# Kernel optimization log

Measured on AMD Instinct MI355X. Metric: run time of the kernel, lower is better.

## Reference

```python
import jax, jax.numpy as jnp
import numpy as np
from jax import lax

H, W = 4096, 4096

def setup_inputs() -> dict:
    key = jax.random.key(0)
    k_occ, k_seed = jax.random.split(key)
    occupied = (jax.random.uniform(k_occ, (H, W)) < 0.3).astype(jnp.float32)
    flood = ((jax.random.uniform(k_seed, (H, W)) < 1e-3).astype(jnp.float32)
             * (1.0 - occupied))
    flood_input = jnp.stack([occupied, flood], axis=-1)  # [H, W, 2]
    flood_count = jnp.zeros((H, W), dtype=jnp.float32)
    # Fixed flood kernel, HWIO layout: (3, 3, in=2, out=1)
    kernel = jnp.zeros((3, 3, 2, 1), dtype=jnp.float32)
    kernel = kernel.at[1, 1, 0, 0].set(-5.0)  # occupied center blocks flood
    kernel = kernel.at[1, 2, 1, 0].set(1.0)   # right
    kernel = kernel.at[2, 1, 1, 0].set(1.0)   # down
    kernel = kernel.at[1, 0, 1, 0].set(1.0)   # left
    kernel = kernel.at[0, 1, 1, 0].set(1.0)   # up
    kernel = kernel.at[1, 1, 1, 0].set(1.0)   # center
    bias = jnp.zeros((1,), dtype=jnp.float32)
    return {"flood_input": flood_input, "flood_count": flood_count,
            "kernel": kernel, "bias": bias, "num_steps": 16}

def reference(flood_input, flood_count, kernel, bias, num_steps):
    dn = ("NHWC", "HWIO", "NHWC")

    def flood_step(carry, _):
        x, count = carry                      # x: [H, W, 2], count: [H, W]
        occupied = x[..., 0]
        y = lax.conv_general_dilated(x[None], kernel, (1, 1), "SAME",
                                     dimension_numbers=dn)[0, ..., 0] + bias[0]
        y = jnp.clip(y, 0.0, 1.0)             # flooded frontier
        new_x = jnp.stack([occupied, y], axis=-1)
        return (new_x, count + y), None

    (x_final, count_final), _ = lax.scan(flood_step,
                                         (flood_input, flood_count),
                                         None, length=num_steps)
    # [H, W, 3]: occupied, flood, count
    return jnp.concatenate([x_final, count_final[..., None]], axis=-1)
```

## Files before the change

kernel.cpp:

```cpp
#include <hip/hip_runtime.h>


typedef unsigned long long u64;

#define HH 4096
#define WW 4096
#define WPR 64
#define TILE 96
#define HALO 16
#define REG 128
#define NSTEPS 16

__global__ __launch_bounds__(256) void pack_kernel(
    const float* __restrict__ flood_input,
    u64* __restrict__ occP, u64* __restrict__ flP)
{
    const int lane = threadIdx.x & 63;
    const int wv   = threadIdx.x >> 6;
    const int r    = blockIdx.x;
#pragma unroll
    for (int b = 0; b < 2; ++b) {
        float vx[8], vy[8];
#pragma unroll
        for (int j = 0; j < 8; ++j) {
            const int w = wv * 16 + b * 8 + j;
            const float2 v = *(const float2*)(flood_input +
                                ((size_t)r * WW + (w << 6) + lane) * 2);
            vx[j] = v.x; vy[j] = v.y;
        }
#pragma unroll
        for (int j = 0; j < 8; ++j) {
            const int w = wv * 16 + b * 8 + j;
            const u64 om = __ballot(vx[j] > 0.5f);
            const u64 fm = __ballot(vy[j] > 0.5f);
            if (lane == 0) {
                occP[(size_t)r * WPR + w] = om;
                flP [(size_t)r * WPR + w] = fm;
            }
        }
    }
}

__global__ __launch_bounds__(256, 8) void flood_kernel(
    const u64* __restrict__ occP, const u64* __restrict__ flP,
    const float* __restrict__ flood_count,
    float* __restrict__ out)
{
    __shared__ u64 occL[REG * 2];
    __shared__ u64 bufA[REG * 2];
    __shared__ u64 bufB[REG * 2];
    __shared__ u64 cntL[TILE * 2 * 5];

    const int tid  = threadIdx.x;
    const int lane = tid & 63;
    const int wv   = tid >> 6;

    const int tile_r0 = blockIdx.y * TILE;
    const int tile_c0 = blockIdx.x * TILE;
    const int row0 = tile_r0 - HALO;
    const int col0 = tile_c0 - HALO;

    const int r  = tid >> 1, h = tid & 1;
    const int gr = row0 + r;
    const bool rin = (gr >= 0) & (gr < HH);
    const int s  = col0 + (h << 6);
    const int q0 = ((s + 64) >> 6) - 1;
    const int sh = s - (q0 << 6);

    const size_t base = (size_t)(rin ? gr : 0) * WPR;
    const int qa = min(max(q0, 0), WPR - 1);
    const int qb = min(max(q0 + 1, 0), WPR - 1);
    u64 o0 = occP[base + qa], o1 = occP[base + qb];
    u64 f0 = flP [base + qa], f1 = flP [base + qb];
    const bool va = rin & (q0 >= 0);
    const bool vb = rin & (q0 + 1 < WPR);
    if (!va) { o0 = ~0ull; f0 = 0ull; }
    if (!vb) { o1 = ~0ull; f1 = 0ull; }
    const u64 occ = (o0 >> sh) | (sh ? (o1 << (64 - sh)) : 0ull);
    u64       f   = (f0 >> sh) | (sh ? (f1 << (64 - sh)) : 0ull);

    occL[tid] = occ;
    bufA[tid] = f;
    __syncthreads();

    u64 cnt0 = 0, cnt1 = 0, cnt2 = 0, cnt3 = 0, cnt4 = 0;
    const u64 nocc = ~occ;
    u64* cur = bufA;
    u64* nxt = bufB;
    for (int it = 0; it < NSTEPS; ++it) {
        const u64 up = (r > 0)       ? cur[tid - 2] : 0ull;
        const u64 dn = (r < REG - 1) ? cur[tid + 2] : 0ull;
        const u64 nb = cur[tid ^ 1];
        const u64 cl = h ? (nb >> 63) : 0ull;
        const u64 cr = h ? 0ull : (nb << 63);
        const u64 nf = nocc & (f | (f << 1) | cl | (f >> 1) | cr | up | dn);
        u64 c = nf, t;
        t = cnt0; cnt0 = t ^ c; c = t & c;
        t = cnt1; cnt1 = t ^ c; c = t & c;
        t = cnt2; cnt2 = t ^ c; c = t & c;
        t = cnt3; cnt3 = t ^ c; c = t & c;
        cnt4 ^= c;
        nxt[tid] = nf;
        f = nf;
        __syncthreads();
        u64* tmp = cur; cur = nxt; nxt = tmp;
    }

    if (r >= HALO && r < HALO + TILE) {
        const int rr = r - HALO;
        u64* c = &cntL[(rr * 2 + h) * 5];
        c[0] = cnt0; c[1] = cnt1; c[2] = cnt2; c[3] = cnt3; c[4] = cnt4;
    }
    __syncthreads();

#pragma unroll 2
    for (int orow = wv; orow < TILE; orow += 4) {
        const int grr = tile_r0 + orow;
        if (grr >= HH) continue;
        const int gc0 = tile_c0 + lane;
        const int gc1 = tile_c0 + 64 + lane;
        const bool v0 = gc0 < WW;
        const bool v1 = (lane < 32) && (gc1 < WW);
        const float fc0 = v0 ? flood_count[(size_t)grr * WW + gc0] : 0.f;
        const float fc1 = v1 ? flood_count[(size_t)grr * WW + gc1] : 0.f;
        const int rreg = orow + HALO;
#pragma unroll
        for (int sp = 0; sp < 2; ++sp) {
            const bool vv = sp ? v1 : v0;
            if (!vv) continue;
            const int oc  = (sp << 6) + lane;
            const int gc  = sp ? gc1 : gc0;
            const int creg = oc + HALO;
            const int word = creg >> 6, bit = creg & 63;
            const u64 ow = occL[rreg * 2 + word];
            const u64 fw = cur [rreg * 2 + word];
            const u64* cp = &cntL[(orow * 2 + word) * 5];
            int cv = 0;
#pragma unroll
            for (int k = 0; k < 5; ++k)
                cv += (int)((cp[k] >> bit) & 1ull) << k;
            float3 o3;
            o3.x = (float)((ow >> bit) & 1ull);
            o3.y = (float)((fw >> bit) & 1ull);
            o3.z = (float)cv + (sp ? fc1 : fc0);
            *(float3*)(out + ((size_t)grr * WW + gc) * 3) = o3;
        }
    }
}

extern "C" void kernel_launch(void* const* d_in, const int* in_sizes, int n_in,
                              void* d_out, int out_size, void* d_ws, size_t ws_size,
                              hipStream_t stream) {
    const float* flood_input = (const float*)d_in[0];
    const float* flood_cnt   = (const float*)d_in[1];
    float* out = (float*)d_out;

    u64* occP = (u64*)d_ws;
    u64* flP  = occP + (size_t)HH * WPR;

    pack_kernel<<<dim3(HH), dim3(256), 0, stream>>>(flood_input, occP, flP);

    dim3 grid((WW + TILE - 1) / TILE, (HH + TILE - 1) / TILE);
    flood_kernel<<<grid, dim3(256), 0, stream>>>(occP, flP, flood_cnt, out);
}
```

Measured before the change: 381.9 us.

## Split flood into column-strip bit-plane kernel and separate expand kernel

Measured after the change: 389.5 us. No clear change (+2.0%).

```diff
diff --git a/kernel.cpp b/kernel.cpp
--- a/kernel.cpp
+++ b/kernel.cpp
@@ -6,14 +6,12 @@
 #define HH 4096
 #define WW 4096
 #define WPR 64
-#define TILE 96
-#define HALO 16
-#define REG 128
 #define NSTEPS 16
+#define VROWS 224
+#define RROWS 256
 
 __global__ __launch_bounds__(256) void pack_kernel(
-    const float* __restrict__ flood_input,
-    u64* __restrict__ occP, u64* __restrict__ flP)
+    const float* __restrict__ in, u64* __restrict__ occP, u64* __restrict__ flP)
 {
     const int lane = threadIdx.x & 63;
     const int wv   = threadIdx.x >> 6;
@@ -24,8 +22,7 @@
 #pragma unroll
         for (int j = 0; j < 8; ++j) {
             const int w = wv * 16 + b * 8 + j;
-            const float2 v = *(const float2*)(flood_input +
-                                ((size_t)r * WW + (w << 6) + lane) * 2);
+            const float2 v = *(const float2*)(in + ((size_t)r * WW + (w << 6) + lane) * 2);
             vx[j] = v.x; vy[j] = v.y;
         }
 #pragma unroll
@@ -34,117 +31,116 @@
             const u64 om = __ballot(vx[j] > 0.5f);
             const u64 fm = __ballot(vy[j] > 0.5f);
             if (lane == 0) {
-                occP[(size_t)r * WPR + w] = om;
-                flP [(size_t)r * WPR + w] = fm;
+                occP[(size_t)w * HH + r] = om;
+                flP [(size_t)w * HH + r] = fm;
             }
         }
     }
 }
 
-__global__ __launch_bounds__(256, 8) void flood_kernel(
+__global__ __launch_bounds__(256) void flood_kernel(
     const u64* __restrict__ occP, const u64* __restrict__ flP,
-    const float* __restrict__ flood_count,
-    float* __restrict__ out)
+    u64* __restrict__ planes)
 {
-    __shared__ u64 occL[REG * 2];
-    __shared__ u64 bufA[REG * 2];
-    __shared__ u64 bufB[REG * 2];
-    __shared__ u64 cntL[TILE * 2 * 5];
+    __shared__ u64 bufA[RROWS * 2];
+    __shared__ u64 bufB[RROWS * 2];
 
-    const int tid  = threadIdx.x;
-    const int lane = tid & 63;
-    const int wv   = tid >> 6;
+    const int tid = threadIdx.x;
+    const int w   = blockIdx.x;
+    const int gr  = blockIdx.y * VROWS + tid - 16;
+    const bool rin = (gr >= 0) && (gr < HH);
 
-    const int tile_r0 = blockIdx.y * TILE;
-    const int tile_c0 = blockIdx.x * TILE;
-    const int row0 = tile_r0 - HALO;
-    const int col0 = tile_c0 - HALO;
+    u64 oc[3], fl[3];
+#pragma unroll
+    for (int j = 0; j < 3; ++j) {
+        const int q = w - 1 + j;
+        const bool v = rin && (q >= 0) && (q < WPR);
+        oc[j] = v ? occP[(size_t)q * HH + gr] : ~0ull;
+        fl[j] = v ? flP [(size_t)q * HH + gr] : 0ull;
+    }
+    const u64 nocc0 = ~((oc[0] >> 48) | (oc[1] << 16));
+    const u64 nocc1 = ~((oc[1] >> 48) | (oc[2] << 16));
+    u64 f0 = (fl[0] >> 48) | (fl[1] << 16);
+    u64 f1 = (fl[1] >> 48) | (fl[2] << 16);
 
-    const int r  = tid >> 1, h = tid & 1;
-    const int gr = row0 + r;
-    const bool rin = (gr >= 0) & (gr < HH);
-    const int s  = col0 + (h << 6);
-    const int q0 = ((s + 64) >> 6) - 1;
-    const int sh = s - (q0 << 6);
+    u64 c00 = 0, c01 = 0, c02 = 0, c03 = 0, c04 = 0;
+    u64 c10 = 0, c11 = 0, c12 = 0, c13 = 0, c14 = 0;
 
-    const size_t base = (size_t)(rin ? gr : 0) * WPR;
-    const int qa = min(max(q0, 0), WPR - 1);
-    const int qb = min(max(q0 + 1, 0), WPR - 1);
-    u64 o0 = occP[base + qa], o1 = occP[base + qb];
-    u64 f0 = flP [base + qa], f1 = flP [base + qb];
-    const bool va = rin & (q0 >= 0);
-    const bool vb = rin & (q0 + 1 < WPR);
-    if (!va) { o0 = ~0ull; f0 = 0ull; }
-    if (!vb) { o1 = ~0ull; f1 = 0ull; }
-    const u64 occ = (o0 >> sh) | (sh ? (o1 << (64 - sh)) : 0ull);
-    u64       f   = (f0 >> sh) | (sh ? (f1 << (64 - sh)) : 0ull);
-
-    occL[tid] = occ;
-    bufA[tid] = f;
+    bufA[tid * 2 + 0] = f0; bufA[tid * 2 + 1] = f1;
     __syncthreads();
 
-    u64 cnt0 = 0, cnt1 = 0, cnt2 = 0, cnt3 = 0, cnt4 = 0;
-    const u64 nocc = ~occ;
     u64* cur = bufA;
     u64* nxt = bufB;
     for (int it = 0; it < NSTEPS; ++it) {
-        const u64 up = (r > 0)       ? cur[tid - 2] : 0ull;
-        const u64 dn = (r < REG - 1) ? cur[tid + 2] : 0ull;
-        const u64 nb = cur[tid ^ 1];
-        const u64 cl = h ? (nb >> 63) : 0ull;
-        const u64 cr = h ? 0ull : (nb << 63);
-        const u64 nf = nocc & (f | (f << 1) | cl | (f >> 1) | cr | up | dn);
-        u64 c = nf, t;
-        t = cnt0; cnt0 = t ^ c; c = t & c;
-        t = cnt1; cnt1 = t ^ c; c = t & c;
-        t = cnt2; cnt2 = t ^ c; c = t & c;
-        t = cnt3; cnt3 = t ^ c; c = t & c;
-        cnt4 ^= c;
-        nxt[tid] = nf;
-        f = nf;
+        u64 up0 = 0, up1 = 0, dn0 = 0, dn1 = 0;
+        if (tid > 0)         { up0 = cur[(tid - 1) * 2 + 0]; up1 = cur[(tid - 1) * 2 + 1]; }
+        if (tid < RROWS - 1) { dn0 = cur[(tid + 1) * 2 + 0]; dn1 = cur[(tid + 1) * 2 + 1]; }
+        const u64 nf0 = nocc0 & (f0 | (f0 << 1) | (f0 >> 1) | (f1 << 63) | up0 | dn0);
+        const u64 nf1 = nocc1 & (f1 | (f1 << 1) | (f0 >> 63) | (f1 >> 1) | up1 | dn1);
+        u64 c, t;
+        c = nf0;
+        t = c00; c00 = t ^ c; c = t & c;
+        t = c01; c01 = t ^ c; c = t & c;
+        t = c02; c02 = t ^ c; c = t & c;
+        t = c03; c03 = t ^ c; c = t & c;
+        c04 ^= c;
+        c = nf1;
+        t = c10; c10 = t ^ c; c = t & c;
+        t = c11; c11 = t ^ c; c = t & c;
+        t = c12; c12 = t ^ c; c = t & c;
+        t = c13; c13 = t ^ c; c = t & c;
+        c14 ^= c;
+        nxt[tid * 2 + 0] = nf0; nxt[tid * 2 + 1] = nf1;
+        f0 = nf0; f1 = nf1;
         __syncthreads();
         u64* tmp = cur; cur = nxt; nxt = tmp;
     }
 
-    if (r >= HALO && r < HALO + TILE) {
-        const int rr = r - HALO;
-        u64* c = &cntL[(rr * 2 + h) * 5];
-        c[0] = cnt0; c[1] = cnt1; c[2] = cnt2; c[3] = cnt3; c[4] = cnt4;
+    if (tid >= 16 && tid < 16 + VROWS && gr < HH) {
+        const size_t o = (size_t)w * HH + gr;
+        const size_t P = (size_t)WPR * HH;
+        planes[o]         = (f0  >> 16) | (f1  << 48);
+        planes[P + o]     = (c00 >> 16) | (c10 << 48);
+        planes[2 * P + o] = (c01 >> 16) | (c11 << 48);
+        planes[3 * P + o] = (c02 >> 16) | (c12 << 48);
+        planes[4 * P + o] = (c03 >> 16) | (c13 << 48);
+        planes[5 * P + o] = (c04 >> 16) | (c14 << 48);
     }
-    __syncthreads();
+}
+
+__global__ __launch_bounds__(256) void expand_kernel(
+    const u64* __restrict__ occP, const u64* __restrict__ planes,
+    const float* __restrict__ fcount, float* __restrict__ out)
+{
+    const int lane = threadIdx.x & 63;
+    const int wv   = threadIdx.x >> 6;
+    const int w    = blockIdx.x;
+    const int r0   = blockIdx.y * 64 + wv * 16;
+    const size_t P = (size_t)WPR * HH;
+    const size_t col = (size_t)(w << 6) + lane;
 
 #pragma unroll 2
-    for (int orow = wv; orow < TILE; orow += 4) {
-        const int grr = tile_r0 + orow;
-        if (grr >= HH) continue;
-        const int gc0 = tile_c0 + lane;
-        const int gc1 = tile_c0 + 64 + lane;
-        const bool v0 = gc0 < WW;
-        const bool v1 = (lane < 32) && (gc1 < WW);
-        const float fc0 = v0 ? flood_count[(size_t)grr * WW + gc0] : 0.f;
-        const float fc1 = v1 ? flood_count[(size_t)grr * WW + gc1] : 0.f;
-        const int rreg = orow + HALO;
-#pragma unroll
-        for (int sp = 0; sp < 2; ++sp) {
-            const bool vv = sp ? v1 : v0;
-            if (!vv) continue;
-            const int oc  = (sp << 6) + lane;
-            const int gc  = sp ? gc1 : gc0;
-            const int creg = oc + HALO;
-            const int word = creg >> 6, bit = creg & 63;
-            const u64 ow = occL[rreg * 2 + word];
-            const u64 fw = cur [rreg * 2 + word];
-            const u64* cp = &cntL[(orow * 2 + word) * 5];
-            int cv = 0;
-#pragma unroll
-            for (int k = 0; k < 5; ++k)
-                cv += (int)((cp[k] >> bit) & 1ull) << k;
-            float3 o3;
-            o3.x = (float)((ow >> bit) & 1ull);
-            o3.y = (float)((fw >> bit) & 1ull);
-            o3.z = (float)cv + (sp ? fc1 : fc0);
-            *(float3*)(out + ((size_t)grr * WW + gc) * 3) = o3;
-        }
+    for (int i = 0; i < 16; ++i) {
+        const int r = r0 + i;
+        const size_t o = (size_t)w * HH + r;
+        const u64 ow = occP[o];
+        const u64 fw = planes[o];
+        const u64 q0 = planes[P + o];
+        const u64 q1 = planes[2 * P + o];
+        const u64 q2 = planes[3 * P + o];
+        const u64 q3 = planes[4 * P + o];
+        const u64 q4 = planes[5 * P + o];
+        const float fc = fcount[(size_t)r * WW + col];
+        const int cv = (int)((q0 >> lane) & 1ull)
+                     + ((int)((q1 >> lane) & 1ull) << 1)
+                     + ((int)((q2 >> lane) & 1ull) << 2)
+                     + ((int)((q3 >> lane) & 1ull) << 3)
+                     + ((int)((q4 >> lane) & 1ull) << 4);
+        float3 o3;
+        o3.x = (float)((ow >> lane) & 1ull);
+        o3.y = (float)((fw >> lane) & 1ull);
+        o3.z = (float)cv + fc;
+        *(float3*)(out + ((size_t)r * WW + col) * 3) = o3;
     }
 }
 
@@ -155,11 +151,13 @@
     const float* flood_cnt   = (const float*)d_in[1];
     float* out = (float*)d_out;
 
-    u64* occP = (u64*)d_ws;
-    u64* flP  = occP + (size_t)HH * WPR;
+    u64* occP   = (u64*)d_ws;
+    u64* flP    = occP + (size_t)WPR * HH;
+    u64* planes = flP  + (size_t)WPR * HH;
 
     pack_kernel<<<dim3(HH), dim3(256), 0, stream>>>(flood_input, occP, flP);
-
-    dim3 grid((WW + TILE - 1) / TILE, (HH + TILE - 1) / TILE);
-    flood_kernel<<<grid, dim3(256), 0, stream>>>(occP, flP, flood_cnt, out);
+    flood_kernel<<<dim3(WPR, (HH + VROWS - 1) / VROWS), dim3(256), 0, stream>>>(
+        occP, flP, planes);
+    expand_kernel<<<dim3(WPR, HH / 64), dim3(256), 0, stream>>>(
+        occP, planes, flood_cnt, out);
 }
```
